# Kernel optimization log

Measured on AMD Instinct MI355X. Metric: run time of the kernel, lower is better.

The kernel has to match this reference:

```python
import jax, jax.numpy as jnp
import numpy as np

N, E, HIN, H, FC, C, G = 50000, 1600000, 7, 128, 256, 2, 512

def _glorot(k, shape):
    fan = shape[0] + shape[1]
    return jax.random.uniform(k, shape, jnp.float32, -1.0, 1.0) * jnp.sqrt(6.0 / fan)

def setup_inputs() -> dict:
    key = jax.random.key(0)
    ks = jax.random.split(key, 40)
    inp = {}
    inp['x'] = jax.random.normal(ks[0], (N, HIN), jnp.float32)
    inp['edge_index'] = jax.random.randint(ks[1], (2, E), 0, N)
    inp['batch'] = jnp.sort(jax.random.randint(ks[2], (N,), 0, G))
    dims = [(HIN, H), (H, H), (H, H)]
    for i, (di, do) in enumerate(dims):
        kk = jax.random.split(ks[3 + i], 3)
        inp[f'Wl{i}'] = _glorot(kk[0], (di, do))
        inp[f'bl{i}'] = jnp.zeros((do,), jnp.float32)
        inp[f'Wr{i}'] = _glorot(kk[1], (di, do))
        inp[f'br{i}'] = jnp.zeros((do,), jnp.float32)
        inp[f'att{i}'] = _glorot(kk[2], (1, do))[0]  # GATv2 att vector [H]
        inp[f'bo{i}'] = jnp.zeros((do,), jnp.float32)
    inp['fc1_W'] = _glorot(ks[10], (H, FC))
    inp['fc1_b'] = jnp.zeros((FC,), jnp.float32)
    inp['fc2_W'] = _glorot(ks[11], (FC, C))
    inp['fc2_b'] = jnp.zeros((C,), jnp.float32)
    return inp

def reference(x, edge_index, batch,
              Wl0, bl0, Wr0, br0, att0, bo0,
              Wl1, bl1, Wr1, br1, att1, bo1,
              Wl2, bl2, Wr2, br2, att2, bo2,
              fc1_W, fc1_b, fc2_W, fc2_b):
    n = x.shape[0]
    loop = jnp.arange(n)
    src = jnp.concatenate([edge_index[0], loop])  # self-loops (PyG default)
    dst = jnp.concatenate([edge_index[1], loop])

    def conv(h, Wl, bl, Wr, br, att, bo):
        xl = h @ Wl + bl               # [N,H] source transform
        xr = h @ Wr + br               # [N,H] target transform
        m = jax.nn.leaky_relu(xl[src] + xr[dst], 0.2)  # [E+N,H]
        e = m @ att                    # [E+N] attention logits
        emax = jax.ops.segment_max(e, dst, num_segments=n)
        w = jnp.exp(e - emax[dst])
        denom = jax.ops.segment_sum(w, dst, num_segments=n)
        alpha = w / denom[dst]         # per-target softmax
        return jax.ops.segment_sum(alpha[:, None] * xl[src], dst, num_segments=n) + bo

    h = jax.nn.elu(conv(x, Wl0, bl0, Wr0, br0, att0, bo0))
    h = jax.nn.elu(conv(h, Wl1, bl1, Wr1, br1, att1, bo1))
    h = jax.nn.elu(conv(h, Wl2, bl2, Wr2, br2, att2, bo2))

    # global_mean_pool
    sums = jax.ops.segment_sum(h, batch, num_segments=G)
    cnt = jax.ops.segment_sum(jnp.ones((n,), h.dtype), batch, num_segments=G)
    g = sums / jnp.maximum(cnt, 1.0)[:, None]

    z = jax.nn.relu(g @ fc1_W + fc1_b)
    logits = z @ fc2_W + fc2_b
    return jax.nn.log_softmax(logits, axis=1)
```

## Files before the change

### kernel.cpp

```cpp
#include <hip/hip_runtime.h>
#include <hip/hip_fp16.h>
#include <math.h>

#define H 128
#define FCD 256
#define BUKSH 7
#define MAXBUK 512

typedef _Float16 half8 __attribute__((ext_vector_type(8)));
typedef float floatx4 __attribute__((ext_vector_type(4)));

template<int CTRL>
__device__ __forceinline__ float dppadd(float x){
  return x + __int_as_float(__builtin_amdgcn_update_dpp(
      0, __float_as_int(x), CTRL, 0xf, 0xf, true));
}
__device__ __forceinline__ float grp16_sum(float x){
  x = dppadd<0x128>(x);
  x = dppadd<0x124>(x);
  x = dppadd<0x122>(x);
  x = dppadd<0x121>(x);
  return x;
}

__global__ void k_scan512(const int* __restrict__ in, int nb,
                          int* __restrict__ out1, int* __restrict__ out2){
  int t = threadIdx.x, lane = t & 63, w = t >> 6;
  int v = (t<nb) ? in[t] : 0;
  int x = v;
  #pragma unroll
  for (int off=1; off<64; off<<=1){
    int y = __shfl_up(x, off);
    if (lane >= off) x += y;
  }
  __shared__ int ws[8];
  if (lane==63) ws[w] = x;
  __syncthreads();
  int wo = 0;
  #pragma unroll
  for (int i=0;i<8;i++) if (i<w) wo += ws[i];
  int excl = wo + x - v;
  if (t<nb){ out1[t] = excl; if (out2) out2[t] = excl; }
  if (t==511) out1[nb] = wo + x;
}

__global__ void k_bhist(const int* __restrict__ ei, int E, int Et, int nbuk,
                        int* __restrict__ bhist){
  __shared__ int lh[MAXBUK];
  int t = threadIdx.x;
  lh[t] = 0;
  __syncthreads();
  int j0 = blockIdx.x*8192;
  #pragma unroll
  for (int i=0;i<16;i++){
    int j = j0 + i*512 + t;
    if (j < Et){
      int dst = (j < E) ? ei[E+j] : (j - E);
      atomicAdd(&lh[dst>>BUKSH], 1);
    }
  }
  __syncthreads();
  if (t < nbuk && lh[t]) atomicAdd(&bhist[t], lh[t]);
}

__global__ void k_bscatter(const int* __restrict__ ei, int E, int Et, int nbuk,
                           int* __restrict__ bnext, unsigned* __restrict__ ebuf){
  __shared__ int lh[MAXBUK];
  __shared__ int lbase[MAXBUK];
  int t = threadIdx.x;
  lh[t] = 0;
  __syncthreads();
  int j0 = blockIdx.x*8192;
  unsigned pk[16]; int bk[16]; int rk[16];
  #pragma unroll
  for (int i=0;i<16;i++){
    int j = j0 + i*512 + t;
    if (j < Et){
      int src, dst;
      if (j < E){ src = ei[j]; dst = ei[E+j]; } else { src = dst = j - E; }
      pk[i] = (unsigned)src | ((unsigned)dst << 16);
      bk[i] = dst >> BUKSH;
      rk[i] = atomicAdd(&lh[bk[i]], 1);
    }
  }
  __syncthreads();
  if (t < nbuk){
    int c = lh[t];
    lbase[t] = c ? atomicAdd(&bnext[t], c) : 0;
  }
  __syncthreads();
  #pragma unroll
  for (int i=0;i<16;i++){
    int j = j0 + i*512 + t;
    if (j < Et) ebuf[lbase[bk[i]] + rk[i]] = pk[i];
  }
}

__global__ void k_bfill(const unsigned* __restrict__ ebuf, const int* __restrict__ bbase,
                        int N, int Et,
                        int* __restrict__ row_ptr, int* __restrict__ deg,
                        int* __restrict__ csr, int* __restrict__ histsT){
  __shared__ int cnt[1<<BUKSH];
  __shared__ int lnxt[1<<BUKSH];
  __shared__ int bh[256];
  __shared__ int ws0[1];
  int b = blockIdx.x, t = threadIdx.x;
  if (t < (1<<BUKSH)) cnt[t] = 0;
  bh[t] = 0;
  if (b==0 && t==0) row_ptr[N] = Et;
  __syncthreads();
  int lo = bbase[b], hi = bbase[b+1];
  for (int j = lo + t; j < hi; j += 256){
    unsigned d = ebuf[j] >> 16;
    atomicAdd(&cnt[d & ((1<<BUKSH)-1)], 1);
  }
  __syncthreads();
  int lane = t & 63;
  int v = (t < (1<<BUKSH)) ? cnt[t] : 0;
  int x = v;
  #pragma unroll
  for (int off=1; off<64; off<<=1){
    int y = __shfl_up(x, off);
    if (lane >= off) x += y;
  }
  if (t==63) ws0[0] = x;
  __syncthreads();
  if (t >= 64 && t < 128) x += ws0[0];
  if (t < (1<<BUKSH)){
    int node = (b<<BUKSH) + t;
    int excl = lo + x - v;
    lnxt[t] = excl;
    if (node < N){
      row_ptr[node] = excl;
      deg[node] = v;
      atomicAdd(&bh[min(v,255)], 1);
    }
  }
  __syncthreads();
  histsT[t*MAXBUK + b] = bh[t];
  for (int j = lo + t; j < hi; j += 256){
    unsigned e = ebuf[j];
    int d = (e >> 16) & ((1<<BUKSH)-1);
    int r = atomicAdd(&lnxt[d], 1);
    csr[r] = e & 0xffff;
  }
}

__global__ void k_dbinscan(int* __restrict__ histsT, int nb, int* __restrict__ bintot){
  int d = blockIdx.x;
  int t = threadIdx.x, lane = t & 63, w = t >> 6;
  int v = (t<nb) ? histsT[d*MAXBUK + t] : 0;
  int x = v;
  #pragma unroll
  for (int off=1; off<64; off<<=1){
    int y = __shfl_up(x, off);
    if (lane >= off) x += y;
  }
  __shared__ int ws[8];
  if (lane==63) ws[w] = x;
  __syncthreads();
  int wo = 0;
  #pragma unroll
  for (int i=0;i<8;i++) if (i<w) wo += ws[i];
  if (t<nb) histsT[d*MAXBUK + t] = wo + x - v;
  if (t==511) bintot[d] = wo + x;
}

__global__ void k_dscatter2(const int* __restrict__ deg, int N,
                            const int* __restrict__ histsT, const int* __restrict__ base,
                            int* __restrict__ perm){
  __shared__ int lh[256];
  int t = threadIdx.x, b = blockIdx.x;
  lh[t] = 0; lh[t+128] = 0;
  __syncthreads();
  int i = (b<<BUKSH) + t;
  if (i < N){
    int d = min(deg[i],255);
    int r = atomicAdd(&lh[d], 1);
    perm[base[d] + histsT[d*MAXBUK + b] + r] = i;
  }
}

__global__ void k_prep(const float* __restrict__ Wl1, const float* __restrict__ Wr1,
                       const float* __restrict__ Wl2, const float* __restrict__ Wr2,
                       _Float16* __restrict__ Wt){
  int idx = blockIdx.x*256 + threadIdx.x;
  int L   = idx >> 15;
  int rem = idx & 32767;
  int nn  = rem >> 7;
  int k   = rem & 127;
  const float* W = (L==0) ? (nn<H?Wl1:Wr1) : (nn<H?Wl2:Wr2);
  Wt[idx] = (_Float16)W[k*H + (nn&127)];
}

__global__ void k_gemm7(const float* __restrict__ x,
                        const float* __restrict__ Wl, const float* __restrict__ bl,
                        const float* __restrict__ Wr, const float* __restrict__ br,
                        __half* __restrict__ xl, __half* __restrict__ xr, int n){
  int col = threadIdx.x;
  int n0 = blockIdx.x*8;
  float accl[8], accr[8];
  float bL = bl[col], bR = br[col];
  #pragma unroll
  for (int t=0;t<8;t++){ accl[t]=bL; accr[t]=bR; }
  #pragma unroll
  for (int k=0;k<7;k++){
    float wl = Wl[k*H + col];
    float wr = Wr[k*H + col];
    #pragma unroll
    for (int t=0;t<8;t++){
      int node = n0+t; if (node >= n) node = n-1;
      float hv = x[(size_t)node*7 + k];
      accl[t] = fmaf(hv, wl, accl[t]);
      accr[t] = fmaf(hv, wr, accr[t]);
    }
  }
  #pragma unroll
  for (int t=0;t<8;t++){
    int node = n0+t;
    if (node < n){
      xl[(size_t)node*H + col] = __float2half(accl[t]);
      xr[(size_t)node*H + col] = __float2half(accr[t]);
    }
  }
}

__global__ __launch_bounds__(256) void k_gemm2h(
    const __half* __restrict__ h, const _Float16* __restrict__ Wt,
    const float* __restrict__ bl, const float* __restrict__ br,
    __half* __restrict__ xl, __half* __restrict__ xr, int n){
  int wave = threadIdx.x >> 6, lane = threadIdx.x & 63;
  int m16 = lane & 15, quad = lane >> 4;
  int row0 = blockIdx.x*64 + wave*16;
  int arow = row0 + m16; if (arow >= n) arow = n-1;
  const __half* hr = h + (size_t)arow*H;
  half8 a[4];
  #pragma unroll
  for (int kb=0;kb<4;kb++) a[kb] = *(const half8*)(hr + kb*32 + quad*8);
  floatx4 acc[16];
  #pragma unroll
  for (int t=0;t<16;t++){ floatx4 z = {0.f,0.f,0.f,0.f}; acc[t] = z; }
  #pragma unroll
  for (int nt=0;nt<16;nt++){
    const _Float16* wr_ = Wt + (size_t)(nt*16 + m16)*H;
    #pragma unroll
    for (int kb=0;kb<4;kb++){
      half8 b = *(const half8*)(wr_ + kb*32 + quad*8);
      acc[nt] = __builtin_amdgcn_mfma_f32_16x16x32_f16(a[kb], b, acc[nt], 0,0,0);
    }
  }
  #pragma unroll
  for (int nt=0;nt<16;nt++){
    int c = nt*16 + m16;
    float bias; __half* dst; int cc;
    if (c < H){ bias = bl[c];   dst = xl; cc = c;   }
    else      { bias = br[c-H]; dst = xr; cc = c-H; }
    #pragma unroll
    for (int r=0;r<4;r++){
      int rw = row0 + quad*4 + r;
      if (rw < n) dst[(size_t)rw*H + cc] = __float2half(acc[nt][r] + bias);
    }
  }
}

__global__ void k_gat(const __half* __restrict__ xl, const __half* __restrict__ xr,
                      const float* __restrict__ att, const float* __restrict__ bo,
                      const int* __restrict__ row_ptr, const int* __restrict__ csr_src,
                      const int* __restrict__ perm,
                      __half* __restrict__ hout, int n){
  int gid0 = (int)((blockIdx.x*blockDim.x + threadIdx.x) >> 4);
  int lane16 = threadIdx.x & 15;
  if (gid0 >= n) return;
  int gid = perm[gid0];
  int f = lane16*8;
  float xrv[8], av[8];
  {
    union { float4 q; __half2 h[4]; } U;
    U.q = *(const float4*)(xr + (size_t)gid*H + f);
    #pragma unroll
    for (int i=0;i<4;i++){ float2 t2 = __half22float2(U.h[i]); xrv[2*i]=t2.x; xrv[2*i+1]=t2.y; }
    float4 a0 = *(const float4*)(att + f);
    float4 a1 = *(const float4*)(att + f + 4);
    av[0]=a0.x; av[1]=a0.y; av[2]=a0.z; av[3]=a0.w;
    av[4]=a1.x; av[5]=a1.y; av[6]=a1.z; av[7]=a1.w;
  }
  float acc[8];
  #pragma unroll
  for (int i=0;i<8;i++) acc[i]=0.f;
  float mmax = -INFINITY, denom = 0.f;
  int beg = row_ptr[gid], end = row_ptr[gid+1];
  int j = beg;
  for (; j+7 < end; j += 8){
    int s[8];
    #pragma unroll
    for (int u=0;u<8;u++) s[u] = csr_src[j+u];
    float4 r[8];
    #pragma unroll
    for (int u=0;u<8;u++) r[u] = *(const float4*)(xl + (size_t)s[u]*H + f);
    float d[8];
    #pragma unroll
    for (int u=0;u<8;u++){
      union { float4 q; __half2 h[4]; } U; U.q = r[u];
      float dd = 0.f;
      #pragma unroll
      for (int i=0;i<4;i++){
        float2 vf = __half22float2(U.h[i]);
        float u0 = vf.x + xrv[2*i];
        float u1 = vf.y + xrv[2*i+1];
        float l0 = fmaf(0.4f, fabsf(u0), 0.6f*u0);
        float l1 = fmaf(0.4f, fabsf(u1), 0.6f*u1);
        dd = fmaf(l0, av[2*i], fmaf(l1, av[2*i+1], dd));
      }
      d[u] = dd;
    }
    #pragma unroll
    for (int u=0;u<8;u++) d[u] = grp16_sum(d[u]);
    float m8 = fmaxf(fmaxf(fmaxf(d[0],d[1]), fmaxf(d[2],d[3])),
                     fmaxf(fmaxf(d[4],d[5]), fmaxf(d[6],d[7])));
    if (m8 > mmax){
      float sc = __expf(mmax - m8);
      #pragma unroll
      for (int i=0;i<8;i++) acc[i] *= sc;
      denom *= sc;
      mmax = m8;
    }
    #pragma unroll
    for (int u=0;u<8;u++){
      float w = __expf(d[u] - mmax);
      denom += w;
      union { float4 q; __half2 h[4]; } U; U.q = r[u];
      #pragma unroll
      for (int i=0;i<4;i++){
        float2 vf = __half22float2(U.h[i]);
        acc[2*i]   = fmaf(w, vf.x, acc[2*i]);
        acc[2*i+1] = fmaf(w, vf.y, acc[2*i+1]);
      }
    }
  }
  for (; j<end; j++){
    int s0 = csr_src[j];
    union { float4 q; __half2 h[4]; } U;
    U.q = *(const float4*)(xl + (size_t)s0*H + f);
    float v0[8];
    #pragma unroll
    for (int i=0;i<4;i++){ float2 t0 = __half22float2(U.h[i]); v0[2*i]=t0.x; v0[2*i+1]=t0.y; }
    float dd = 0.f;
    #pragma unroll
    for (int i=0;i<8;i++){
      float u0 = v0[i] + xrv[i];
      float l0 = fmaf(0.4f, fabsf(u0), 0.6f*u0);
      dd = fmaf(l0, av[i], dd);
    }
    dd = grp16_sum(dd);
    if (dd > mmax){
      float sc = __expf(mmax - dd);
      #pragma unroll
      for (int i=0;i<8;i++) acc[i] *= sc;
      denom *= sc;
      mmax = dd;
    }
    float w = __expf(dd - mmax);
    denom += w;
    #pragma unroll
    for (int i=0;i<8;i++) acc[i] = fmaf(w, v0[i], acc[i]);
  }
  float inv = 1.f/denom;
  float o[8];
  {
    float4 b0 = *(const float4*)(bo + f);
    float4 b1 = *(const float4*)(bo + f + 4);
    float bb[8] = {b0.x,b0.y,b0.z,b0.w,b1.x,b1.y,b1.z,b1.w};
    #pragma unroll
    for (int i=0;i<8;i++){
      float t = acc[i]*inv + bb[i];
      o[i] = t > 0.f ? t : expm1f(t);
    }
  }
  union { float4 f4; __half2 h2[4]; } u;
  #pragma unroll
  for (int i=0;i<4;i++) u.h2[i] = __floats2half2_rn(o[2*i], o[2*i+1]);
  *(float4*)(hout + (size_t)gid*H + f) = u.f4;
}

__global__ void k_fc(const __half* __restrict__ hbuf, const int* __restrict__ batch, int N,
                     const float* __restrict__ W1, const float* __restrict__ b1,
                     const float* __restrict__ W2, const float* __restrict__ b2,
                     float* __restrict__ out){
  __shared__ float g[H];
  __shared__ float2 part[4][64];
  __shared__ float zs[FCD];
  __shared__ int bounds[2];
  int gi = blockIdx.x;
  int t = threadIdx.x;
  if (t < 2){
    int target = gi + t;
    int lo = 0, hi = N;
    while (lo < hi){ int mid = (lo+hi)>>1; if (batch[mid] < target) lo = mid+1; else hi = mid; }
    bounds[t] = lo;
  }
  __syncthreads();
  int lo = bounds[0], hi = bounds[1];
  int pairc = t & 63, slice = t >> 6;
  float sx = 0.f, sy = 0.f;
  for (int node = lo + slice; node < hi; node += 4){
    float2 f2 = __half22float2(*(const __half2*)(hbuf + (size_t)node*H + pairc*2));
    sx += f2.x; sy += f2.y;
  }
  part[slice][pairc] = make_float2(sx, sy);
  __syncthreads();
  if (t < 64){
    float2 a = part[0][t], b = part[1][t], c = part[2][t], d = part[3][t];
    float cnt = (float)(hi - lo); if (cnt < 1.f) cnt = 1.f;
    float inv = 1.f/cnt;
    g[2*t]   = (a.x+b.x+c.x+d.x)*inv;
    g[2*t+1] = (a.y+b.y+c.y+d.y)*inv;
  }
  __syncthreads();
  float acc = b1[t];
  for (int k=0;k<H;k++) acc = fmaf(g[k], W1[k*FCD+t], acc);
  zs[t] = acc > 0.f ? acc : 0.f;
  __syncthreads();
  if (t < 2){
    float l = b2[t];
    for (int k=0;k<FCD;k++) l = fmaf(zs[k], W2[k*2+t], l);
    g[t] = l;
  }
  __syncthreads();
  if (t < 2){
    float l0 = g[0], l1 = g[1];
    float mx = fmaxf(l0,l1);
    float lse = mx + logf(__expf(l0-mx) + __expf(l1-mx));
    out[gi*2+t] = g[t] - lse;
  }
}

extern "C" void kernel_launch(void* const* d_in, const int* in_sizes, int n_in,
                              void* d_out, int out_size, void* d_ws, size_t ws_size,
                              hipStream_t stream) {
  const float* x     = (const float*)d_in[0];
  const int*   ei    = (const int*)  d_in[1];
  const int*   batch = (const int*)  d_in[2];
  const float* Wl[3]  = {(const float*)d_in[3],  (const float*)d_in[9],  (const float*)d_in[15]};
  const float* bl[3]  = {(const float*)d_in[4],  (const float*)d_in[10], (const float*)d_in[16]};
  const float* Wr[3]  = {(const float*)d_in[5],  (const float*)d_in[11], (const float*)d_in[17]};
  const float* br[3]  = {(const float*)d_in[6],  (const float*)d_in[12], (const float*)d_in[18]};
  const float* att[3] = {(const float*)d_in[7],  (const float*)d_in[13], (const float*)d_in[19]};
  const float* bo[3]  = {(const float*)d_in[8],  (const float*)d_in[14], (const float*)d_in[20]};
  const float* fc1W = (const float*)d_in[21];
  const float* fc1b = (const float*)d_in[22];
  const float* fc2W = (const float*)d_in[23];
  const float* fc2b = (const float*)d_in[24];

  const int N  = in_sizes[2];
  const int E  = in_sizes[1]/2;
  const int Et = E + N;
  const int G  = out_size/2;
  const int NBUK = (N + (1<<BUKSH)-1) >> BUKSH;
  const int NEB = (Et + 8191)/8192;

  char* p = (char*)d_ws;
  auto alloc = [&](size_t bytes)->void*{
    void* r = (void*)p; p += (bytes + 255) & ~(size_t)255; return r;
  };
  int*      deg     = (int*)     alloc((size_t)N*4);
  int*      row_ptr = (int*)     alloc((size_t)(N+1)*4);
  int*      bhist   = (int*)     alloc((size_t)(MAXBUK+1)*4);
  int*      bbase   = (int*)     alloc((size_t)(MAXBUK+1)*4);
  int*      bnext   = (int*)     alloc((size_t)(MAXBUK+1)*4);
  int*      histsT  = (int*)     alloc((size_t)256*MAXBUK*4);
  int*      bintot  = (int*)     alloc((size_t)260*4);
  int*      dbase   = (int*)     alloc((size_t)260*4);
  int*      perm    = (int*)     alloc((size_t)N*4);
  int*      csr     = (int*)     alloc((size_t)Et*4);
  unsigned* ebuf    = (unsigned*)alloc((size_t)Et*4);
  __half*   xl      = (__half*)  alloc((size_t)N*H*2);
  __half*   xr      = (__half*)  alloc((size_t)N*H*2);
  __half*   hbuf    = (__half*)  alloc((size_t)N*H*2);
  _Float16* Wt      = (_Float16*)alloc((size_t)2*256*H*2);

  (void)hipMemsetAsync(bhist, 0, (size_t)(MAXBUK+1)*4, stream);
  k_prep<<<256, 256, 0, stream>>>(Wl[1], Wr[1], Wl[2], Wr[2], Wt);

  k_bhist   <<<NEB, 512, 0, stream>>>(ei, E, Et, NBUK, bhist);
  k_scan512 <<<1, 512, 0, stream>>>(bhist, NBUK, bbase, bnext);
  k_bscatter<<<NEB, 512, 0, stream>>>(ei, E, Et, NBUK, bnext, ebuf);
  k_bfill   <<<NBUK, 256, 0, stream>>>(ebuf, bbase, N, Et, row_ptr, deg, csr, histsT);
  k_dbinscan<<<256, 512, 0, stream>>>(histsT, NBUK, bintot);
  k_scan512 <<<1, 512, 0, stream>>>(bintot, 256, dbase, nullptr);
  k_dscatter2<<<NBUK, 128, 0, stream>>>(deg, N, histsT, dbase, perm);

  const int g7  = (N + 7)/8;
  const int gM  = (N + 63)/64;
  const int gg  = (int)(((size_t)N*16 + 255)/256);

  k_gemm7<<<g7, 128, 0, stream>>>(x, Wl[0], bl[0], Wr[0], br[0], xl, xr, N);
  k_gat<<<gg, 256, 0, stream>>>(xl, xr, att[0], bo[0], row_ptr, csr, perm, hbuf, N);
  k_gemm2h<<<gM, 256, 0, stream>>>(hbuf, Wt, bl[1], br[1], xl, xr, N);
  k_gat<<<gg, 256, 0, stream>>>(xl, xr, att[1], bo[1], row_ptr, csr, perm, hbuf, N);
  k_gemm2h<<<gM, 256, 0, stream>>>(hbuf, Wt + (size_t)256*H, bl[2], br[2], xl, xr, N);
  k_gat<<<gg, 256, 0, stream>>>(xl, xr, att[2], bo[2], row_ptr, csr, perm, hbuf, N);

  k_fc<<<G, 256, 0, stream>>>(hbuf, batch, N, fc1W, fc1b, fc2W, fc2b, (float*)d_out);
}
```

Before: 460.6 us.

## Pre-scale CSR offsets, merge scans, fold memset, swizzle weights, simplify leaky-relu

```diff
diff --git a/kernel.cpp b/kernel.cpp
--- a/kernel.cpp
+++ b/kernel.cpp
@@ -142,7 +142,7 @@
     unsigned e = ebuf[j];
     int d = (e >> 16) & ((1<<BUKSH)-1);
     int r = atomicAdd(&lnxt[d], 1);
-    csr[r] = e & 0xffff;
+    csr[r] = (int)((e & 0xffff) << 8);
   }
 }
 
@@ -167,30 +167,53 @@
 }
 
 __global__ void k_dscatter2(const int* __restrict__ deg, int N,
-                            const int* __restrict__ histsT, const int* __restrict__ base,
+                            const int* __restrict__ histsT, const int* __restrict__ bintot,
                             int* __restrict__ perm){
   __shared__ int lh[256];
+  __shared__ int sbase[256];
+  __shared__ int ws[4];
   int t = threadIdx.x, b = blockIdx.x;
-  lh[t] = 0; lh[t+128] = 0;
-  __syncthreads();
-  int i = (b<<BUKSH) + t;
-  if (i < N){
-    int d = min(deg[i],255);
-    int r = atomicAdd(&lh[d], 1);
-    perm[base[d] + histsT[d*MAXBUK + b] + r] = i;
+  int lane = t & 63, w = t >> 6;
+  int v = bintot[t];
+  int x = v;
+  #pragma unroll
+  for (int off=1; off<64; off<<=1){
+    int y = __shfl_up(x, off);
+    if (lane >= off) x += y;
+  }
+  if (lane==63) ws[w] = x;
+  lh[t] = 0;
+  __syncthreads();
+  int wo = (w>0?ws[0]:0) + (w>1?ws[1]:0) + (w>2?ws[2]:0);
+  sbase[t] = wo + x - v;
+  __syncthreads();
+  if (t < 128){
+    int i = (b<<BUKSH) + t;
+    if (i < N){
+      int d = min(deg[i],255);
+      int r = atomicAdd(&lh[d], 1);
+      perm[sbase[d] + histsT[d*MAXBUK + b] + r] = i;
+    }
   }
 }
 
 __global__ void k_prep(const float* __restrict__ Wl1, const float* __restrict__ Wr1,
                        const float* __restrict__ Wl2, const float* __restrict__ Wr2,
-                       _Float16* __restrict__ Wt){
+                       _Float16* __restrict__ Wt, int* __restrict__ bhist){
   int idx = blockIdx.x*256 + threadIdx.x;
-  int L   = idx >> 15;
-  int rem = idx & 32767;
-  int nn  = rem >> 7;
-  int k   = rem & 127;
-  const float* W = (L==0) ? (nn<H?Wl1:Wr1) : (nn<H?Wl2:Wr2);
-  Wt[idx] = (_Float16)W[k*H + (nn&127)];
+  if (blockIdx.x == 0){
+    for (int i = threadIdx.x; i <= MAXBUK; i += 256) bhist[i] = 0;
+  }
+  int e    = idx & 7;
+  int lane = (idx >> 3) & 63;
+  int kb   = (idx >> 9) & 3;
+  int nt   = (idx >> 11) & 15;
+  int L    = idx >> 15;
+  int m16 = lane & 15, quad = lane >> 4;
+  int k = kb*32 + quad*8 + e;
+  int n = nt*16 + m16;
+  const float* W = (L==0) ? (n<H?Wl1:Wr1) : (n<H?Wl2:Wr2);
+  Wt[idx] = (_Float16)W[k*H + (n&127)];
 }
 
 __global__ void k_gemm7(const float* __restrict__ x,
@@ -242,10 +265,10 @@
   for (int t=0;t<16;t++){ floatx4 z = {0.f,0.f,0.f,0.f}; acc[t] = z; }
   #pragma unroll
   for (int nt=0;nt<16;nt++){
-    const _Float16* wr_ = Wt + (size_t)(nt*16 + m16)*H;
+    const _Float16* bp = Wt + ((size_t)nt*4)*512 + lane*8;
     #pragma unroll
     for (int kb=0;kb<4;kb++){
-      half8 b = *(const half8*)(wr_ + kb*32 + quad*8);
+      half8 b = *(const half8*)(bp + kb*512);
       acc[nt] = __builtin_amdgcn_mfma_f32_16x16x32_f16(a[kb], b, acc[nt], 0,0,0);
     }
   }
@@ -271,7 +294,8 @@
   int gid0 = (int)((blockIdx.x*blockDim.x + threadIdx.x) >> 4);
   int lane16 = threadIdx.x & 15;
   if (gid0 >= n) return;
-  int gid = perm[gid0];
+  int gid = perm[n-1-gid0];
+  const char* xlb = (const char*)xl + lane16*16;
   int f = lane16*8;
   float xrv[8], av[8];
   {
@@ -296,22 +320,21 @@
     for (int u=0;u<8;u++) s[u] = csr_src[j+u];
     float4 r[8];
     #pragma unroll
-    for (int u=0;u<8;u++) r[u] = *(const float4*)(xl + (size_t)s[u]*H + f);
+    for (int u=0;u<8;u++) r[u] = *(const float4*)(xlb + s[u]);
     float d[8];
     #pragma unroll
     for (int u=0;u<8;u++){
       union { float4 q; __half2 h[4]; } U; U.q = r[u];
-      float dd = 0.f;
+      float pp = 0.f, qq = 0.f;
       #pragma unroll
       for (int i=0;i<4;i++){
         float2 vf = __half22float2(U.h[i]);
         float u0 = vf.x + xrv[2*i];
         float u1 = vf.y + xrv[2*i+1];
-        float l0 = fmaf(0.4f, fabsf(u0), 0.6f*u0);
-        float l1 = fmaf(0.4f, fabsf(u1), 0.6f*u1);
-        dd = fmaf(l0, av[2*i], fmaf(l1, av[2*i+1], dd));
+        pp = fmaf(u0, av[2*i], pp);  qq = fmaf(fabsf(u0), av[2*i], qq);
+        pp = fmaf(u1, av[2*i+1], pp); qq = fmaf(fabsf(u1), av[2*i+1], qq);
       }
-      d[u] = dd;
+      d[u] = fmaf(0.6f, pp, 0.4f*qq);
     }
     #pragma unroll
     for (int u=0;u<8;u++) d[u] = grp16_sum(d[u]);
@@ -340,17 +363,17 @@
   for (; j<end; j++){
     int s0 = csr_src[j];
     union { float4 q; __half2 h[4]; } U;
-    U.q = *(const float4*)(xl + (size_t)s0*H + f);
+    U.q = *(const float4*)(xlb + s0);
     float v0[8];
     #pragma unroll
     for (int i=0;i<4;i++){ float2 t0 = __half22float2(U.h[i]); v0[2*i]=t0.x; v0[2*i+1]=t0.y; }
-    float dd = 0.f;
+    float pp = 0.f, qq = 0.f;
     #pragma unroll
     for (int i=0;i<8;i++){
       float u0 = v0[i] + xrv[i];
-      float l0 = fmaf(0.4f, fabsf(u0), 0.6f*u0);
-      dd = fmaf(l0, av[i], dd);
-    }
+      pp = fmaf(u0, av[i], pp);  qq = fmaf(fabsf(u0), av[i], qq);
+    }
+    float dd = fmaf(0.6f, pp, 0.4f*qq);
     dd = grp16_sum(dd);
     if (dd > mmax){
       float sc = __expf(mmax - dd);
@@ -469,25 +492,22 @@
   int*      bnext   = (int*)     alloc((size_t)(MAXBUK+1)*4);
   int*      histsT  = (int*)     alloc((size_t)256*MAXBUK*4);
   int*      bintot  = (int*)     alloc((size_t)260*4);
-  int*      dbase   = (int*)     alloc((size_t)260*4);
   int*      perm    = (int*)     alloc((size_t)N*4);
   int*      csr     = (int*)     alloc((size_t)Et*4);
   unsigned* ebuf    = (unsigned*)alloc((size_t)Et*4);
   __half*   xl      = (__half*)  alloc((size_t)N*H*2);
   __half*   xr      = (__half*)  alloc((size_t)N*H*2);
   __half*   hbuf    = (__half*)  alloc((size_t)N*H*2);
-  _Float16* Wt      = (_Float16*)alloc((size_t)2*256*H*2);
-
-  (void)hipMemsetAsync(bhist, 0, (size_t)(MAXBUK+1)*4, stream);
-  k_prep<<<256, 256, 0, stream>>>(Wl[1], Wr[1], Wl[2], Wr[2], Wt);
+  _Float16* Wt      = (_Float16*)alloc((size_t)2*16*4*512*2);
+
+  k_prep<<<256, 256, 0, stream>>>(Wl[1], Wr[1], Wl[2], Wr[2], Wt, bhist);
 
   k_bhist   <<<NEB, 512, 0, stream>>>(ei, E, Et, NBUK, bhist);
   k_scan512 <<<1, 512, 0, stream>>>(bhist, NBUK, bbase, bnext);
   k_bscatter<<<NEB, 512, 0, stream>>>(ei, E, Et, NBUK, bnext, ebuf);
   k_bfill   <<<NBUK, 256, 0, stream>>>(ebuf, bbase, N, Et, row_ptr, deg, csr, histsT);
   k_dbinscan<<<256, 512, 0, stream>>>(histsT, NBUK, bintot);
-  k_scan512 <<<1, 512, 0, stream>>>(bintot, 256, dbase, nullptr);
-  k_dscatter2<<<NBUK, 128, 0, stream>>>(deg, N, histsT, dbase, perm);
+  k_dscatter2<<<NBUK, 256, 0, stream>>>(deg, N, histsT, bintot, perm);
 
   const int g7  = (N + 7)/8;
   const int gM  = (N + 63)/64;
@@ -497,7 +517,7 @@
   k_gat<<<gg, 256, 0, stream>>>(xl, xr, att[0], bo[0], row_ptr, csr, perm, hbuf, N);
   k_gemm2h<<<gM, 256, 0, stream>>>(hbuf, Wt, bl[1], br[1], xl, xr, N);
   k_gat<<<gg, 256, 0, stream>>>(xl, xr, att[1], bo[1], row_ptr, csr, perm, hbuf, N);
-  k_gemm2h<<<gM, 256, 0, stream>>>(hbuf, Wt + (size_t)256*H, bl[2], br[2], xl, xr, N);
+  k_gemm2h<<<gM, 256, 0, stream>>>(hbuf, Wt + (size_t)16*4*512, bl[2], br[2], xl, xr, N);
   k_gat<<<gg, 256, 0, stream>>>(xl, xr, att[2], bo[2], row_ptr, csr, perm, hbuf, N);
 
   k_fc<<<G, 256, 0, stream>>>(hbuf, batch, N, fc1W, fc1b, fc2W, fc2b, (float*)d_out);
```

Measured after the change: 402.4 us. 12.6% less time.
